# Performance work log

Hardware: AMD Instinct MI355X
Metric: run time of the kernel (lower is better)

The kernel has to match this reference:

```python
import jax, jax.numpy as jnp
import numpy as np

B, CB, IN, OUT, K, H = 32, 1, 2048, 2048, 8, 512


def setup_inputs() -> dict:
    key = jax.random.key(0)
    ks = jax.random.split(key, 6)
    return {
        "x": jax.random.normal(ks[0], (B, IN), dtype=jnp.float32),
        "condition": jax.random.normal(ks[1], (CB, IN), dtype=jnp.float32),
        "w1": jax.random.normal(ks[2], (IN, H), dtype=jnp.float32) * 0.02,
        "b1": jnp.zeros((H,), dtype=jnp.float32),
        "w2": jax.random.normal(ks[3], (H, K), dtype=jnp.float32) * 0.02,
        "b2": jnp.zeros((K,), dtype=jnp.float32),
        "kernels_weights": jax.random.normal(ks[4], (K, OUT, IN), dtype=jnp.float32) * 0.01,
        "kernels_bias": jnp.zeros((K, OUT), dtype=jnp.float32),
    }


def reference(x, condition, w1, b1, w2, b2, kernels_weights, kernels_bias):
    # Attention over kernels (temperature = 1).
    # condition: (cond_batch, in); scores: (cond_batch, K)
    scores = jnp.maximum(condition @ w1 + b1, 0.0) @ w2 + b2
    batch = x.shape[0]
    # Original repeats scores over the batch then softmaxes over kernels.
    alphas = jax.nn.softmax(jnp.broadcast_to(scores[None], (batch,) + scores.shape), axis=-1)  # (B, cond_batch, K)
    # The original broadcast multiply-sum only type-checks for cond_batch == 1.
    a = alphas[:, 0, :]  # (B, K)
    # agg_weights = sum_k alpha_bk * W_k : (B, out, in)
    agg_w = jnp.einsum("bk,koi->boi", a, kernels_weights)
    agg_b = jnp.einsum("bk,ko->bo", a, kernels_bias)  # (B, out)
    # Per-sample linear: out_bo = sum_i agg_w[b,o,i] * x[b,i] + agg_b[b,o]
    out = jnp.einsum("boi,bi->bo", agg_w, x) + agg_b
    return out
```

## Files before the change

### kernel.cpp

```cpp
#include <hip/hip_runtime.h>

#define B_SZ  32
#define IN_D  2048
#define OUT_D 2048
#define K_N   8
#define H_D   512
#define NPART 64

__global__ void k1_partial(const float* __restrict__ cond,
                           const float* __restrict__ w1,
                           float* __restrict__ ws) {
    const int m   = blockIdx.x;
    const int tid = threadIdx.x;
    const int ibase = m * (IN_D / NPART);
    float p0 = 0.f, p1 = 0.f;
    for (int ii = 0; ii < IN_D / NPART; ++ii) {
        const float c = cond[ibase + ii];
        const float* row = w1 + (size_t)(ibase + ii) * H_D;
        p0 = fmaf(c, row[tid], p0);
        p1 = fmaf(c, row[tid + 256], p1);
    }
    float* part = ws + 1024;
    part[(size_t)m * H_D + tid]       = p0;
    part[(size_t)m * H_D + tid + 256] = p1;
}

__global__ void k1_scores(const float* __restrict__ b1,
                          const float* __restrict__ w2,
                          const float* __restrict__ b2,
                          float* __restrict__ ws) {
    __shared__ float hsh[H_D];
    const int tid = threadIdx.x;
    const float* part = ws + 1024;
    float acc = b1[tid];
    for (int m = 0; m < NPART; ++m) acc += part[(size_t)m * H_D + tid];
    hsh[tid] = fmaxf(acc, 0.f);
    __syncthreads();
    if (tid < 64) {
        float s[K_N];
        #pragma unroll
        for (int k = 0; k < K_N; ++k) s[k] = 0.f;
        #pragma unroll
        for (int jj = 0; jj < H_D / 64; ++jj) {
            const int j = jj * 64 + tid;
            const float hv = hsh[j];
            const float* wr = w2 + (size_t)j * K_N;
            #pragma unroll
            for (int k = 0; k < K_N; ++k) s[k] = fmaf(hv, wr[k], s[k]);
        }
        #pragma unroll
        for (int k = 0; k < K_N; ++k) {
            #pragma unroll
            for (int d = 1; d < 64; d <<= 1) s[k] += __shfl_xor(s[k], d, 64);
        }
        if (tid == 0) {
            float mx = -1e30f;
            #pragma unroll
            for (int k = 0; k < K_N; ++k) { s[k] += b2[k]; mx = fmaxf(mx, s[k]); }
            float sum = 0.f;
            #pragma unroll
            for (int k = 0; k < K_N; ++k) { s[k] = __expf(s[k] - mx); sum += s[k]; }
            const float inv = 1.f / sum;
            #pragma unroll
            for (int k = 0; k < K_N; ++k) ws[k] = s[k] * inv;
        }
    }
}

__global__ __launch_bounds__(256, 4) void k2_main(
    const float* __restrict__ x,
    const float* __restrict__ kw,
    const float* __restrict__ kb,
    const float* __restrict__ ws,
    float* __restrict__ out) {
    __shared__ float red[B_SZ][257];
    __shared__ float fin[8][B_SZ];
    const int tid = threadIdx.x;
    const int o0  = blockIdx.x * 2;
    const int i0  = tid * 8;

    float a[K_N];
    #pragma unroll
    for (int k = 0; k < K_N; ++k) a[k] = ws[k];

    float wa[8], wb[8];
    #pragma unroll
    for (int j = 0; j < 8; ++j) { wa[j] = 0.f; wb[j] = 0.f; }
    #pragma unroll
    for (int k = 0; k < K_N; ++k) {
        const float* p = kw + ((size_t)k * OUT_D + o0) * IN_D + i0;
        float wv[8], wv2[8];
        *(float4*)&wv[0]  = *(const float4*)(p);
        *(float4*)&wv[4]  = *(const float4*)(p + 4);
        *(float4*)&wv2[0] = *(const float4*)(p + IN_D);
        *(float4*)&wv2[4] = *(const float4*)(p + IN_D + 4);
        const float ak = a[k];
        #pragma unroll
        for (int j = 0; j < 8; ++j) {
            wa[j] = fmaf(ak, wv[j],  wa[j]);
            wb[j] = fmaf(ak, wv2[j], wb[j]);
        }
    }

    float acc0[B_SZ], acc1[B_SZ];
    #pragma unroll
    for (int b = 0; b < B_SZ; ++b) {
        const float* xp = x + (size_t)b * IN_D + i0;
        float xv[8];
        *(float4*)&xv[0] = *(const float4*)(xp);
        *(float4*)&xv[4] = *(const float4*)(xp + 4);
        float s0 = 0.f, s1 = 0.f;
        #pragma unroll
        for (int j = 0; j < 8; ++j) {
            s0 = fmaf(wa[j], xv[j], s0);
            s1 = fmaf(wb[j], xv[j], s1);
        }
        acc0[b] = s0; acc1[b] = s1;
    }

    const int r = tid >> 5;
    const int b = tid & 31;

    #pragma unroll
    for (int j = 0; j < B_SZ; ++j) red[j][tid] = acc0[j];
    __syncthreads();
    {
        float s = 0.f;
        #pragma unroll
        for (int c = 0; c < 32; ++c) s += red[b][r * 32 + c];
        fin[r][b] = s;
    }
    __syncthreads();
    if (tid < B_SZ) {
        float tot = 0.f;
        #pragma unroll
        for (int rr = 0; rr < 8; ++rr) tot += fin[rr][tid];
        float aggb = 0.f;
        #pragma unroll
        for (int k = 0; k < K_N; ++k) aggb = fmaf(a[k], kb[(size_t)k * OUT_D + o0], aggb);
        out[(size_t)tid * OUT_D + o0] = tot + aggb;
    }
    __syncthreads();

    #pragma unroll
    for (int j = 0; j < B_SZ; ++j) red[j][tid] = acc1[j];
    __syncthreads();
    {
        float s = 0.f;
        #pragma unroll
        for (int c = 0; c < 32; ++c) s += red[b][r * 32 + c];
        fin[r][b] = s;
    }
    __syncthreads();
    if (tid < B_SZ) {
        float tot = 0.f;
        #pragma unroll
        for (int rr = 0; rr < 8; ++rr) tot += fin[rr][tid];
        float aggb = 0.f;
        #pragma unroll
        for (int k = 0; k < K_N; ++k) aggb = fmaf(a[k], kb[(size_t)k * OUT_D + o0 + 1], aggb);
        out[(size_t)tid * OUT_D + o0 + 1] = tot + aggb;
    }
}

extern "C" void kernel_launch(void* const* d_in, const int* in_sizes, int n_in,
                              void* d_out, int out_size, void* d_ws, size_t ws_size,
                              hipStream_t stream) {
    (void)in_sizes; (void)n_in; (void)out_size; (void)ws_size;
    const float* x    = (const float*)d_in[0];
    const float* cond = (const float*)d_in[1];
    const float* w1   = (const float*)d_in[2];
    const float* b1   = (const float*)d_in[3];
    const float* w2   = (const float*)d_in[4];
    const float* b2   = (const float*)d_in[5];
    const float* kw   = (const float*)d_in[6];
    const float* kb   = (const float*)d_in[7];
    float* out = (float*)d_out;
    float* ws  = (float*)d_ws;

    k1_partial<<<NPART, 256, 0, stream>>>(cond, w1, ws);
    k1_scores<<<1, H_D, 0, stream>>>(b1, w2, b2, ws);
    k2_main<<<OUT_D / 2, 256, 0, stream>>>(x, kw, kb, ws, out);
}
```

Baseline: 222.7 us.

## Process one output row per block and parallelize score reduction across waves

The main kernel now assigns one output row per block instead of two and launches twice as many blocks. This halves per-thread register arrays (accumulators and weight sums), which should lift occupancy and improve latency hiding for the 128 MB weight stream. The cost is that the x tile is reloaded twice as often overall. The scores kernel now has all 512 threads do the w2 multiply with per-wave shuffle reductions plus a small shared reduction, and some loops gain unroll pragmas.

```diff
diff --git a/kernel.cpp b/kernel.cpp
--- a/kernel.cpp
+++ b/kernel.cpp
@@ -10,10 +10,11 @@
 __global__ void k1_partial(const float* __restrict__ cond,
                            const float* __restrict__ w1,
                            float* __restrict__ ws) {
-    const int m   = blockIdx.x;
-    const int tid = threadIdx.x;
+    const int m     = blockIdx.x;
+    const int tid   = threadIdx.x;
     const int ibase = m * (IN_D / NPART);
     float p0 = 0.f, p1 = 0.f;
+    #pragma unroll
     for (int ii = 0; ii < IN_D / NPART; ++ii) {
         const float c = cond[ibase + ii];
         const float* row = w1 + (size_t)(ibase + ii) * H_D;
@@ -29,41 +30,48 @@
                           const float* __restrict__ w2,
                           const float* __restrict__ b2,
                           float* __restrict__ ws) {
-    __shared__ float hsh[H_D];
+    __shared__ float sred[8][K_N];
     const int tid = threadIdx.x;
     const float* part = ws + 1024;
     float acc = b1[tid];
+    #pragma unroll
     for (int m = 0; m < NPART; ++m) acc += part[(size_t)m * H_D + tid];
-    hsh[tid] = fmaxf(acc, 0.f);
+    const float h = fmaxf(acc, 0.f);
+
+    const float* wr = w2 + (size_t)tid * K_N;
+    float s[K_N];
+    #pragma unroll
+    for (int k = 0; k < K_N; ++k) s[k] = h * wr[k];
+
+    #pragma unroll
+    for (int k = 0; k < K_N; ++k) {
+        #pragma unroll
+        for (int d = 1; d < 64; d <<= 1) s[k] += __shfl_xor(s[k], d, 64);
+    }
+    if ((tid & 63) == 0) {
+        const int w = tid >> 6;
+        #pragma unroll
+        for (int k = 0; k < K_N; ++k) sred[w][k] = s[k];
+    }
     __syncthreads();
-    if (tid < 64) {
-        float s[K_N];
-        #pragma unroll
-        for (int k = 0; k < K_N; ++k) s[k] = 0.f;
-        #pragma unroll
-        for (int jj = 0; jj < H_D / 64; ++jj) {
-            const int j = jj * 64 + tid;
-            const float hv = hsh[j];
-            const float* wr = w2 + (size_t)j * K_N;
-            #pragma unroll
-            for (int k = 0; k < K_N; ++k) s[k] = fmaf(hv, wr[k], s[k]);
-        }
+    if (tid == 0) {
+        float sc[K_N];
         #pragma unroll
         for (int k = 0; k < K_N; ++k) {
+            float v = b2[k];
             #pragma unroll
-            for (int d = 1; d < 64; d <<= 1) s[k] += __shfl_xor(s[k], d, 64);
+            for (int w = 0; w < 8; ++w) v += sred[w][k];
+            sc[k] = v;
         }
-        if (tid == 0) {
-            float mx = -1e30f;
-            #pragma unroll
-            for (int k = 0; k < K_N; ++k) { s[k] += b2[k]; mx = fmaxf(mx, s[k]); }
-            float sum = 0.f;
-            #pragma unroll
-            for (int k = 0; k < K_N; ++k) { s[k] = __expf(s[k] - mx); sum += s[k]; }
-            const float inv = 1.f / sum;
-            #pragma unroll
-            for (int k = 0; k < K_N; ++k) ws[k] = s[k] * inv;
-        }
+        float mx = -1e30f;
+        #pragma unroll
+        for (int k = 0; k < K_N; ++k) mx = fmaxf(mx, sc[k]);
+        float sum = 0.f;
+        #pragma unroll
+        for (int k = 0; k < K_N; ++k) { sc[k] = __expf(sc[k] - mx); sum += sc[k]; }
+        const float inv = 1.f / sum;
+        #pragma unroll
+        for (int k = 0; k < K_N; ++k) ws[k] = sc[k] * inv;
     }
 }
 
@@ -74,57 +82,48 @@
     const float* __restrict__ ws,
     float* __restrict__ out) {
     __shared__ float red[B_SZ][257];
-    __shared__ float fin[8][B_SZ];
+    __shared__ float fin[8][33];
     const int tid = threadIdx.x;
-    const int o0  = blockIdx.x * 2;
+    const int o   = blockIdx.x;
     const int i0  = tid * 8;
 
     float a[K_N];
     #pragma unroll
     for (int k = 0; k < K_N; ++k) a[k] = ws[k];
 
-    float wa[8], wb[8];
+    float wa[8];
     #pragma unroll
-    for (int j = 0; j < 8; ++j) { wa[j] = 0.f; wb[j] = 0.f; }
+    for (int j = 0; j < 8; ++j) wa[j] = 0.f;
     #pragma unroll
     for (int k = 0; k < K_N; ++k) {
-        const float* p = kw + ((size_t)k * OUT_D + o0) * IN_D + i0;
-        float wv[8], wv2[8];
-        *(float4*)&wv[0]  = *(const float4*)(p);
-        *(float4*)&wv[4]  = *(const float4*)(p + 4);
-        *(float4*)&wv2[0] = *(const float4*)(p + IN_D);
-        *(float4*)&wv2[4] = *(const float4*)(p + IN_D + 4);
+        const float* p = kw + ((size_t)k * OUT_D + o) * IN_D + i0;
+        float wv[8];
+        *(float4*)&wv[0] = *(const float4*)(p);
+        *(float4*)&wv[4] = *(const float4*)(p + 4);
         const float ak = a[k];
         #pragma unroll
-        for (int j = 0; j < 8; ++j) {
-            wa[j] = fmaf(ak, wv[j],  wa[j]);
-            wb[j] = fmaf(ak, wv2[j], wb[j]);
-        }
+        for (int j = 0; j < 8; ++j) wa[j] = fmaf(ak, wv[j], wa[j]);
     }
 
-    float acc0[B_SZ], acc1[B_SZ];
+    float acc[B_SZ];
     #pragma unroll
     for (int b = 0; b < B_SZ; ++b) {
         const float* xp = x + (size_t)b * IN_D + i0;
         float xv[8];
         *(float4*)&xv[0] = *(const float4*)(xp);
         *(float4*)&xv[4] = *(const float4*)(xp + 4);
-        float s0 = 0.f, s1 = 0.f;
+        float s = 0.f;
         #pragma unroll
-        for (int j = 0; j < 8; ++j) {
-            s0 = fmaf(wa[j], xv[j], s0);
-            s1 = fmaf(wb[j], xv[j], s1);
-        }
-        acc0[b] = s0; acc1[b] = s1;
+        for (int j = 0; j < 8; ++j) s = fmaf(wa[j], xv[j], s);
+        acc[b] = s;
     }
 
-    const int r = tid >> 5;
-    const int b = tid & 31;
-
     #pragma unroll
-    for (int j = 0; j < B_SZ; ++j) red[j][tid] = acc0[j];
+    for (int j = 0; j < B_SZ; ++j) red[j][tid] = acc[j];
     __syncthreads();
     {
+        const int r = tid >> 5;
+        const int b = tid & 31;
         float s = 0.f;
         #pragma unroll
         for (int c = 0; c < 32; ++c) s += red[b][r * 32 + c];
@@ -137,29 +136,8 @@
         for (int rr = 0; rr < 8; ++rr) tot += fin[rr][tid];
         float aggb = 0.f;
         #pragma unroll
-        for (int k = 0; k < K_N; ++k) aggb = fmaf(a[k], kb[(size_t)k * OUT_D + o0], aggb);
-        out[(size_t)tid * OUT_D + o0] = tot + aggb;
-    }
-    __syncthreads();
-
-    #pragma unroll
-    for (int j = 0; j < B_SZ; ++j) red[j][tid] = acc1[j];
-    __syncthreads();
-    {
-        float s = 0.f;
-        #pragma unroll
-        for (int c = 0; c < 32; ++c) s += red[b][r * 32 + c];
-        fin[r][b] = s;
-    }
-    __syncthreads();
-    if (tid < B_SZ) {
-        float tot = 0.f;
-        #pragma unroll
-        for (int rr = 0; rr < 8; ++rr) tot += fin[rr][tid];
-        float aggb = 0.f;
-        #pragma unroll
-        for (int k = 0; k < K_N; ++k) aggb = fmaf(a[k], kb[(size_t)k * OUT_D + o0 + 1], aggb);
-        out[(size_t)tid * OUT_D + o0 + 1] = tot + aggb;
+        for (int k = 0; k < K_N; ++k) aggb = fmaf(a[k], kb[(size_t)k * OUT_D + o], aggb);
+        out[(size_t)tid * OUT_D + o] = tot + aggb;
     }
 }
 
@@ -180,5 +158,5 @@
 
     k1_partial<<<NPART, 256, 0, stream>>>(cond, w1, ws);
     k1_scores<<<1, H_D, 0, stream>>>(b1, w2, b2, ws);
-    k2_main<<<OUT_D / 2, 256, 0, stream>>>(x, kw, kb, ws, out);
+    k2_main<<<OUT_D, 256, 0, stream>>>(x, kw, kb, ws, out);
 }
```

Result: no change. 226.3 us (+1.6%).
